# Performance work log

Measured on AMD Instinct MI355X. Metric: run time of the kernel, lower is better.

The kernel has to match this reference:

```python
import jax, jax.numpy as jnp
import numpy as np

B, LM, LX, D = 16, 1024, 1024, 768


def setup_inputs() -> dict:
    key = jax.random.key(0)
    k1, k2, k3, k4 = jax.random.split(key, 4)
    main = jax.random.normal(k1, (B, LM, D), dtype=jnp.float32)
    x = jax.random.normal(k2, (B, LX, D), dtype=jnp.float32)
    # keras 'uniform' init ~ U(-0.05, 0.05); scale to keep activations sane
    W = jax.random.uniform(k3, (D, D), dtype=jnp.float32, minval=-0.05, maxval=0.05)
    w = jax.random.uniform(k4, (2 * D, 1), dtype=jnp.float32, minval=-0.05, maxval=0.05)
    return {"main": main, "x": x, "W": W, "w": w}


def reference(main, x, W, w):
    # bilinear co-attention scores: (main @ W) . x^T -> (B, LM, LX)
    proj = jnp.einsum('bmd,de->bme', main, W)            # (B, LM, D)
    scores = jnp.einsum('bme,bne->bmn', proj, x)         # (B, LM, LX) -- no softmax in original
    A = jnp.einsum('bmn,bnd->bmd', scores, x)            # attended features (B, LM, D)
    s = main - A
    m = main * A
    outputs = jnp.concatenate([s, m], axis=-1)           # (B, LM, 2D)
    beta = jnp.einsum('bmk,k->bm', outputs, w[:, 0])     # (B, LM) -- raw, no softmax
    pooled = jnp.einsum('bm,bmk->bk', beta, outputs)     # weighted-sum pooling (B, 2D)
    return pooled
```

## Files before the change

kernel.cpp:

```cpp
#include <hip/hip_runtime.h>

constexpr int kB  = 16;
constexpr int kLM = 1024;
constexpr int kLX = 1024;
constexpr int kD  = 768;

using short8 = __attribute__((ext_vector_type(8))) short;
using f32x4  = __attribute__((ext_vector_type(4))) float;

__device__ __forceinline__ unsigned short f2bf(float f) {
    unsigned u = __float_as_uint(f);
    u = (u + 0x7FFF + ((u >> 16) & 1)) >> 16;
    return (unsigned short)u;
}
__device__ __forceinline__ float bf2f(unsigned short h) {
    return __uint_as_float(((unsigned)h) << 16);
}

__device__ __forceinline__ void gl_lds16(const unsigned short* g, unsigned short* l) {
    auto gp = (const __attribute__((address_space(1))) unsigned int*)g;
    auto lp = (__attribute__((address_space(3))) unsigned int*)l;
    __builtin_amdgcn_global_load_lds(gp, lp, 16, 0, 0);
}

__global__ __launch_bounds__(256) void transpose_cvt_kernel(
    const float* __restrict__ x, unsigned short* __restrict__ xT) {
    __shared__ float tile[64][65];
    const int b  = blockIdx.z;
    const int l0 = blockIdx.x * 64;
    const int d0 = blockIdx.y * 64;
    const int t  = threadIdx.x;
    const int tx = t & 15, ty = t >> 4;
    const float* xb = x + ((size_t)b * kLX + l0) * kD + d0;
#pragma unroll
    for (int p = 0; p < 4; ++p) {
        int r = p * 16 + ty;
        float4 v = *(const float4*)(xb + (size_t)r * kD + tx * 4);
        *(float4*)&tile[r][tx * 4] = v;
    }
    __syncthreads();
    unsigned short* xTb = xT + ((size_t)b * kD + d0) * kLX + l0;
#pragma unroll
    for (int p = 0; p < 4; ++p) {
        int dr = p * 16 + ty;
        ushort4 o;
        o.x = f2bf(tile[tx * 4 + 0][dr]);
        o.y = f2bf(tile[tx * 4 + 1][dr]);
        o.z = f2bf(tile[tx * 4 + 2][dr]);
        o.w = f2bf(tile[tx * 4 + 3][dr]);
        *(ushort4*)(xTb + (size_t)dr * kLX + tx * 4) = o;
    }
}

__global__ __launch_bounds__(256) void cvt_bf16_kernel(
    const float* __restrict__ in, unsigned short* __restrict__ out, int n4) {
    int i = blockIdx.x * blockDim.x + threadIdx.x;
    if (i < n4) {
        float4 v = ((const float4*)in)[i];
        ushort4 o;
        o.x = f2bf(v.x); o.y = f2bf(v.y); o.z = f2bf(v.z); o.w = f2bf(v.w);
        ((ushort4*)out)[i] = o;
    }
}

__global__ __launch_bounds__(256) void gemm_nt_bf16_kernel(
    const unsigned short* __restrict__ A, const unsigned short* __restrict__ B,
    unsigned short* __restrict__ C, int M, int N, int K,
    long sA, long sB, long sC) {
    __shared__ unsigned short Asm[128 * 32];
    __shared__ unsigned short Bsm[128 * 32];
    const int b  = blockIdx.z;
    const int i0 = blockIdx.x * 128;
    const int j0 = blockIdx.y * 128;
    const int t    = threadIdx.x;
    const int wave = t >> 6, lane = t & 63;
    const int wr = (wave >> 1) * 64, wc = (wave & 1) * 64;
    const int quad = lane >> 4, l15 = lane & 15;

    const unsigned short* Ab = A + (size_t)b * sA + (size_t)i0 * K;
    const unsigned short* Bb = B + (size_t)b * sB + (size_t)j0 * K;

    const int c0 = wave * 64 + lane;
    const int c1 = 256 + wave * 64 + lane;
    auto chunk_off = [&](int c) -> size_t {
        int sr = c >> 3, s = c & 7;
        int tt = s ^ (sr & 7);
        int r  = sr * 2 + (tt >> 2);
        int q  = tt & 3;
        return (size_t)r * K + q * 8;
    };
    const size_t off0 = chunk_off(c0);
    const size_t off1 = chunk_off(c1);

    const int sfr = ((l15 & 1) * 4 + quad) ^ ((l15 >> 1) & 7);
    const unsigned short* aP = Asm + ((wr >> 1) * 64 + (l15 >> 1) * 64 + sfr * 8);
    const unsigned short* bP = Bsm + ((wc >> 1) * 64 + (l15 >> 1) * 64 + sfr * 8);

    f32x4 acc[4][4];
    const f32x4 z = {0.f, 0.f, 0.f, 0.f};
#pragma unroll
    for (int i = 0; i < 4; ++i)
#pragma unroll
        for (int j = 0; j < 4; ++j) acc[i][j] = z;

    for (int k0 = 0; k0 < K; k0 += 32) {
        __syncthreads();
        gl_lds16(Ab + off0 + k0, Asm + c0 * 8);
        gl_lds16(Ab + off1 + k0, Asm + c1 * 8);
        gl_lds16(Bb + off0 + k0, Bsm + c0 * 8);
        gl_lds16(Bb + off1 + k0, Bsm + c1 * 8);
        __syncthreads();
        short8 af[4], bg[4];
#pragma unroll
        for (int i = 0; i < 4; ++i) af[i] = *(const short8*)(aP + i * 512);
#pragma unroll
        for (int j = 0; j < 4; ++j) bg[j] = *(const short8*)(bP + j * 512);
#pragma unroll
        for (int i = 0; i < 4; ++i)
#pragma unroll
            for (int j = 0; j < 4; ++j)
                acc[i][j] = __builtin_amdgcn_mfma_f32_16x16x32_bf16(
                    af[i], bg[j], acc[i][j], 0, 0, 0);
    }

    unsigned short* Cb = C + (size_t)b * sC + (size_t)(i0 + wr) * N + j0 + wc;
#pragma unroll
    for (int i = 0; i < 4; ++i)
#pragma unroll
        for (int j = 0; j < 4; ++j)
#pragma unroll
            for (int r = 0; r < 4; ++r)
                Cb[(size_t)(i * 16 + quad * 4 + r) * N + j * 16 + l15] =
                    f2bf(acc[i][j][r]);
}

__global__ __launch_bounds__(256) void pool_kernel(
    const float* __restrict__ mainp, const unsigned short* __restrict__ Aout,
    const float* __restrict__ w, float* __restrict__ out) {
    const int b     = blockIdx.y;
    const int chunk = blockIdx.x;
    const int wave  = threadIdx.x >> 6, lane = threadIdx.x & 63;
    float w1[12], w2[12], ps[12], pm[12];
#pragma unroll
    for (int s = 0; s < 12; ++s) {
        w1[s] = w[s * 64 + lane];
        w2[s] = w[kD + s * 64 + lane];
        ps[s] = 0.f; pm[s] = 0.f;
    }
    for (int rr = 0; rr < 16; ++rr) {
        const int row = chunk * 64 + rr * 4 + wave;
        const float* mr = mainp + ((size_t)b * kLM + row) * kD;
        const unsigned short* ar = Aout + ((size_t)b * kLM + row) * kD;
        float sv[12], mv[12], acc = 0.f;
#pragma unroll
        for (int s = 0; s < 12; ++s) {
            float m_ = mr[s * 64 + lane];
            float a_ = bf2f(ar[s * 64 + lane]);
            sv[s] = m_ - a_;
            mv[s] = m_ * a_;
            acc += sv[s] * w1[s] + mv[s] * w2[s];
        }
#pragma unroll
        for (int off = 32; off; off >>= 1) acc += __shfl_xor(acc, off);
#pragma unroll
        for (int s = 0; s < 12; ++s) { ps[s] += acc * sv[s]; pm[s] += acc * mv[s]; }
    }
    float* ob = out + (size_t)b * 2 * kD;
#pragma unroll
    for (int s = 0; s < 12; ++s) {
        atomicAdd(&ob[s * 64 + lane], ps[s]);
        atomicAdd(&ob[kD + s * 64 + lane], pm[s]);
    }
}

extern "C" void kernel_launch(void* const* d_in, const int* in_sizes, int n_in,
                              void* d_out, int out_size, void* d_ws, size_t ws_size,
                              hipStream_t stream) {
    const float* mainp = (const float*)d_in[0];
    const float* x     = (const float*)d_in[1];
    const float* W     = (const float*)d_in[2];
    const float* w     = (const float*)d_in[3];
    float* out = (float*)d_out;

    char* p = (char*)d_ws;
    unsigned short* xT    = (unsigned short*)p; p += (size_t)kB * kD * kLX * 2;
    unsigned short* mainb = (unsigned short*)p; p += (size_t)kB * kLM * kD * 2;
    unsigned short* Wb    = (unsigned short*)p; p += (size_t)kD * kD * 2;
    unsigned short* G     = (unsigned short*)p; p += (size_t)kB * kD * kD * 2;
    unsigned short* Mt    = (unsigned short*)p; p += (size_t)kB * kD * kD * 2;
    unsigned short* Ao    = (unsigned short*)p; p += (size_t)kB * kLM * kD * 2;

    hipMemsetAsync(out, 0, (size_t)kB * 2 * kD * sizeof(float), stream);

    transpose_cvt_kernel<<<dim3(kLX / 64, kD / 64, kB), 256, 0, stream>>>(x, xT);
    {
        int n4 = kB * kLM * kD / 4;
        cvt_bf16_kernel<<<(n4 + 255) / 256, 256, 0, stream>>>(mainp, mainb, n4);
        n4 = kD * kD / 4;
        cvt_bf16_kernel<<<(n4 + 255) / 256, 256, 0, stream>>>(W, Wb, n4);
    }
    gemm_nt_bf16_kernel<<<dim3(kD / 128, kD / 128, kB), 256, 0, stream>>>(
        xT, xT, G, kD, kD, kLX, (long)kD * kLX, (long)kD * kLX, (long)kD * kD);
    gemm_nt_bf16_kernel<<<dim3(kD / 128, kD / 128, kB), 256, 0, stream>>>(
        G, Wb, Mt, kD, kD, kD, (long)kD * kD, 0L, (long)kD * kD);
    gemm_nt_bf16_kernel<<<dim3(kLM / 128, kD / 128, kB), 256, 0, stream>>>(
        mainb, Mt, Ao, kLM, kD, kD, (long)kLM * kD, (long)kD * kD, (long)kLM * kD);
    pool_kernel<<<dim3(kLM / 64, kB), 256, 0, stream>>>(mainp, Ao, w, out);
}
```

Measured before the change: 256.1 us.

## Double-buffer GEMM LDS tiles, merge bf16 conversions, widen pooling grid

The bf16 GEMM now uses two LDS buffers per operand. It issues the async global-to-LDS loads for the next K tile before running the MFMAs on the current one, and drops one barrier per iteration. This aims to hide global load latency behind matrix math, at the cost of doubled shared memory per block. The two fp32-to-bf16 conversion launches are merged into one kernel. The pooling kernel now handles 16 rows per block instead of 64, giving four times as many blocks but also four times as many atomic adds.

```diff
diff --git a/kernel.cpp b/kernel.cpp
--- a/kernel.cpp
+++ b/kernel.cpp
@@ -52,23 +52,25 @@
     }
 }
 
-__global__ __launch_bounds__(256) void cvt_bf16_kernel(
-    const float* __restrict__ in, unsigned short* __restrict__ out, int n4) {
+__global__ __launch_bounds__(256) void cvt_bf16_dual_kernel(
+    const float* __restrict__ a, unsigned short* __restrict__ oa, int n4a,
+    const float* __restrict__ b, unsigned short* __restrict__ ob, int n4b) {
     int i = blockIdx.x * blockDim.x + threadIdx.x;
-    if (i < n4) {
-        float4 v = ((const float4*)in)[i];
-        ushort4 o;
-        o.x = f2bf(v.x); o.y = f2bf(v.y); o.z = f2bf(v.z); o.w = f2bf(v.w);
-        ((ushort4*)out)[i] = o;
-    }
+    const float* src; unsigned short* dst; int idx;
+    if (i < n4a) { src = a; dst = oa; idx = i; }
+    else { idx = i - n4a; if (idx >= n4b) return; src = b; dst = ob; }
+    float4 v = ((const float4*)src)[idx];
+    ushort4 o;
+    o.x = f2bf(v.x); o.y = f2bf(v.y); o.z = f2bf(v.z); o.w = f2bf(v.w);
+    ((ushort4*)dst)[idx] = o;
 }
 
 __global__ __launch_bounds__(256) void gemm_nt_bf16_kernel(
     const unsigned short* __restrict__ A, const unsigned short* __restrict__ B,
     unsigned short* __restrict__ C, int M, int N, int K,
     long sA, long sB, long sC) {
-    __shared__ unsigned short Asm[128 * 32];
-    __shared__ unsigned short Bsm[128 * 32];
+    __shared__ unsigned short Asm[2][128 * 32];
+    __shared__ unsigned short Bsm[2][128 * 32];
     const int b  = blockIdx.z;
     const int i0 = blockIdx.x * 128;
     const int j0 = blockIdx.y * 128;
@@ -93,8 +95,8 @@
     const size_t off1 = chunk_off(c1);
 
     const int sfr = ((l15 & 1) * 4 + quad) ^ ((l15 >> 1) & 7);
-    const unsigned short* aP = Asm + ((wr >> 1) * 64 + (l15 >> 1) * 64 + sfr * 8);
-    const unsigned short* bP = Bsm + ((wc >> 1) * 64 + (l15 >> 1) * 64 + sfr * 8);
+    const int aOff = (wr >> 1) * 64 + (l15 >> 1) * 64 + sfr * 8;
+    const int bOff = (wc >> 1) * 64 + (l15 >> 1) * 64 + sfr * 8;
 
     f32x4 acc[4][4];
     const f32x4 z = {0.f, 0.f, 0.f, 0.f};
@@ -103,13 +105,26 @@
 #pragma unroll
         for (int j = 0; j < 4; ++j) acc[i][j] = z;
 
-    for (int k0 = 0; k0 < K; k0 += 32) {
+    const int T = K >> 5;
+    gl_lds16(Ab + off0, Asm[0] + c0 * 8);
+    gl_lds16(Ab + off1, Asm[0] + c1 * 8);
+    gl_lds16(Bb + off0, Bsm[0] + c0 * 8);
+    gl_lds16(Bb + off1, Bsm[0] + c1 * 8);
+
+    int buf = 0;
+    for (int kt = 0; kt < T; ++kt) {
         __syncthreads();
-        gl_lds16(Ab + off0 + k0, Asm + c0 * 8);
-        gl_lds16(Ab + off1 + k0, Asm + c1 * 8);
-        gl_lds16(Bb + off0 + k0, Bsm + c0 * 8);
-        gl_lds16(Bb + off1 + k0, Bsm + c1 * 8);
-        __syncthreads();
+        if (kt + 1 < T) {
+            const size_t k = (size_t)(kt + 1) << 5;
+            unsigned short* An = Asm[buf ^ 1];
+            unsigned short* Bn = Bsm[buf ^ 1];
+            gl_lds16(Ab + off0 + k, An + c0 * 8);
+            gl_lds16(Ab + off1 + k, An + c1 * 8);
+            gl_lds16(Bb + off0 + k, Bn + c0 * 8);
+            gl_lds16(Bb + off1 + k, Bn + c1 * 8);
+        }
+        const unsigned short* aP = Asm[buf] + aOff;
+        const unsigned short* bP = Bsm[buf] + bOff;
         short8 af[4], bg[4];
 #pragma unroll
         for (int i = 0; i < 4; ++i) af[i] = *(const short8*)(aP + i * 512);
@@ -121,6 +136,7 @@
             for (int j = 0; j < 4; ++j)
                 acc[i][j] = __builtin_amdgcn_mfma_f32_16x16x32_bf16(
                     af[i], bg[j], acc[i][j], 0, 0, 0);
+        buf ^= 1;
     }
 
     unsigned short* Cb = C + (size_t)b * sC + (size_t)(i0 + wr) * N + j0 + wc;
@@ -147,8 +163,9 @@
         w2[s] = w[kD + s * 64 + lane];
         ps[s] = 0.f; pm[s] = 0.f;
     }
-    for (int rr = 0; rr < 16; ++rr) {
-        const int row = chunk * 64 + rr * 4 + wave;
+#pragma unroll
+    for (int rr = 0; rr < 4; ++rr) {
+        const int row = chunk * 16 + rr * 4 + wave;
         const float* mr = mainp + ((size_t)b * kLM + row) * kD;
         const unsigned short* ar = Aout + ((size_t)b * kLM + row) * kD;
         float sv[12], mv[12], acc = 0.f;
@@ -194,10 +211,10 @@
 
     transpose_cvt_kernel<<<dim3(kLX / 64, kD / 64, kB), 256, 0, stream>>>(x, xT);
     {
-        int n4 = kB * kLM * kD / 4;
-        cvt_bf16_kernel<<<(n4 + 255) / 256, 256, 0, stream>>>(mainp, mainb, n4);
-        n4 = kD * kD / 4;
-        cvt_bf16_kernel<<<(n4 + 255) / 256, 256, 0, stream>>>(W, Wb, n4);
+        int n4a = kB * kLM * kD / 4;
+        int n4b = kD * kD / 4;
+        cvt_bf16_dual_kernel<<<(n4a + n4b + 255) / 256, 256, 0, stream>>>(
+            mainp, mainb, n4a, W, Wb, n4b);
     }
     gemm_nt_bf16_kernel<<<dim3(kD / 128, kD / 128, kB), 256, 0, stream>>>(
         xT, xT, G, kD, kD, kLX, (long)kD * kLX, (long)kD * kLX, (long)kD * kD);
@@ -205,5 +222,5 @@
         G, Wb, Mt, kD, kD, kD, (long)kD * kD, 0L, (long)kD * kD);
     gemm_nt_bf16_kernel<<<dim3(kLM / 128, kD / 128, kB), 256, 0, stream>>>(
         mainb, Mt, Ao, kLM, kD, kD, (long)kLM * kD, (long)kD * kD, (long)kLM * kD);
-    pool_kernel<<<dim3(kLM / 64, kB), 256, 0, stream>>>(mainp, Ao, w, out);
-}
+    pool_kernel<<<dim3(kLM / 16, kB), 256, 0, stream>>>(mainp, Ao, w, out);
+}
```

New measurement: 264.8 us. 1.03x slower.
